# Performance work log

Measured on AMD Instinct MI355X. Metric: run time of the kernel, lower is better.

The kernel has to match this reference:

```python
import jax, jax.numpy as jnp
import numpy as np

B, T, D_MODEL, N_HEADS = 4, 2048, 1024, 16


def _alibi_bias(n_heads, seq_len):
    # matches torch alibi_bias(): slopes 2**(-8*i/m), i=1..m, m = pow2_ceil(n_heads)
    m = 1
    while m < n_heads:
        m *= 2
    slopes = jnp.array([2.0 ** (-8.0 * i / m) for i in range(1, m + 1)][:n_heads],
                       dtype=jnp.float32)
    pos = jnp.arange(seq_len)
    bias = (pos[None, :] - pos[:, None]).astype(jnp.float32)  # [T, T], j - i
    return slopes[:, None, None, None] * bias[None, None]      # [H, 1, T, T]


def setup_inputs() -> dict:
    key = jax.random.key(0)
    kx, kqkv, ko = jax.random.split(key, 3)
    x = jax.random.normal(kx, (B, T, D_MODEL), dtype=jnp.float32)
    Wqkv = jax.random.normal(kqkv, (3 * D_MODEL, D_MODEL), dtype=jnp.float32) / np.sqrt(D_MODEL)
    Wo = jax.random.normal(ko, (D_MODEL, D_MODEL), dtype=jnp.float32) / np.sqrt(D_MODEL)
    alibi = _alibi_bias(N_HEADS, T)  # [H, 1, T, T]
    return {"x": x, "alibi": alibi, "Wqkv": Wqkv, "Wo": Wo}


def reference(x, alibi, Wqkv, Wo):
    Bb, Tt, C = x.shape
    H = N_HEADS
    dk = C // H
    # qkv projection: [B, T, 3C] -> [B, T, 3, H, dk]
    qkv = (x @ Wqkv.T).reshape(Bb, Tt, 3, H, dk)
    q = jnp.moveaxis(qkv[:, :, 0], 2, 1)  # [B, H, T, dk]
    k = jnp.moveaxis(qkv[:, :, 1], 2, 1)
    v = jnp.moveaxis(qkv[:, :, 2], 2, 1)
    # causal (-inf above diagonal) + alibi additive mask, fp32, like the torch path
    causal = jnp.triu(jnp.full((Tt, Tt), -jnp.inf, dtype=jnp.float32), k=1)
    mask = causal[None, None] + alibi[:, 0][None]  # [1, H, T, T]
    scores = jnp.einsum('bhqd,bhkd->bhqk', q, k) / jnp.sqrt(jnp.float32(dk)) + mask
    p = jax.nn.softmax(scores, axis=-1)
    att = jnp.einsum('bhqk,bhkd->bhqd', p, v)           # [B, H, T, dk]
    y = jnp.moveaxis(att, 1, 2).reshape(Bb, Tt, C)       # [B, T, C]
    return y @ Wo.T
```

## Files before the change

kernel.cpp:

```cpp
#include <hip/hip_runtime.h>
#include <hip/hip_bf16.h>


#define B_ 4
#define T_ 2048
#define C_ 1024
#define H_ 16
#define DK 64

typedef __attribute__((ext_vector_type(8))) short short8;
typedef __attribute__((ext_vector_type(4))) float floatx4;

#define GLDS16(g, l)                                                          \
    __builtin_amdgcn_global_load_lds(                                         \
        (const __attribute__((address_space(1))) void*)(g),                   \
        (__attribute__((address_space(3))) void*)(l), 16, 0, 0)

static __device__ inline short f2bf(float x) {
    __hip_bfloat16 h = __float2bfloat16(x);
    return *reinterpret_cast<short*>(&h);
}

__global__ void detect_k(const unsigned int* __restrict__ x,
                         const unsigned int* __restrict__ ali,
                         const unsigned int* __restrict__ wqkv,
                         const unsigned int* __restrict__ wo,
                         int* __restrict__ flags) {
    __shared__ int cnt[4];
    const int tid = threadIdx.x;
    if (tid < 4) cnt[tid] = 0;
    __syncthreads();
    const int g = tid >> 6, l = tid & 63;
    const unsigned int* p = (g == 0) ? x : (g == 1) ? ali : (g == 2) ? wqkv : wo;
    int c = 0;
    for (int i = 0; i < 4; i++) {
        unsigned int w = p[l * 4 + i];
        int e0 = (w >> 7) & 0xFF;
        int e1 = (w >> 23) & 0xFF;
        c += (e0 >= 100 && e0 <= 140);
        c += (e1 >= 100 && e1 <= 140);
    }
    atomicAdd(&cnt[g], c);
    __syncthreads();
    if (l == 0) flags[g] = (cnt[g] < 400) ? 1 : 0;
}

__global__ void tobf16_all_k(const void* __restrict__ x,
                             const void* __restrict__ wq,
                             const void* __restrict__ wo,
                             short* __restrict__ ox,
                             short* __restrict__ owq,
                             short* __restrict__ owo) {
    const int bid = blockIdx.x;
    const void* in;
    short* out;
    int n8, b0, nb;
    if (bid < 2048) {
        in = x; out = ox; n8 = B_ * T_ * C_ / 8; b0 = bid; nb = 2048;
    } else if (bid < 3584) {
        in = wq; out = owq; n8 = 3 * C_ * C_ / 8; b0 = bid - 2048; nb = 1536;
    } else {
        in = wo; out = owo; n8 = C_ * C_ / 8; b0 = bid - 3584; nb = 512;
    }
    const unsigned int* u = (const unsigned int*)in;
    int c = 0;
#pragma unroll
    for (int i = 0; i < 16; i++) {
        unsigned int w = u[i];
        int e0 = (w >> 7) & 0xFF;
        int e1 = (w >> 23) & 0xFF;
        c += (e0 >= 100 && e0 <= 140);
        c += (e1 >= 100 && e1 <= 140);
    }
    const bool f32 = (c < 25);
    int i = b0 * blockDim.x + threadIdx.x;
    const int stride = nb * blockDim.x;
    for (; i < n8; i += stride) {
        if (f32) {
            float4 f0 = ((const float4*)in)[2 * i];
            float4 f1 = ((const float4*)in)[2 * i + 1];
            short8 v = { f2bf(f0.x), f2bf(f0.y), f2bf(f0.z), f2bf(f0.w),
                         f2bf(f1.x), f2bf(f1.y), f2bf(f1.z), f2bf(f1.w) };
            *(short8*)(out + (size_t)i * 8) = v;
        } else {
            *(short8*)(out + (size_t)i * 8) = ((const short8*)in)[i];
        }
    }
}

__global__ __launch_bounds__(256) void gemm_qkvvt_k(
    const short* __restrict__ xbf, const short* __restrict__ wqkvbf,
    short* __restrict__ qkv) {
    const int K = 1024;
    const int tid  = threadIdx.x;
    const int wv   = tid >> 6;
    const int lane = tid & 63;
    const int l15  = lane & 15;
    const int quad = lane >> 4;
    const int wm = wv >> 1, wn = wv & 1;

    const int id = blockIdx.x;
    const bool m0 = id < 1024;
    int bm, bn;
    const short *Ap, *Wp;
    if (m0) {
        bn = id & 15; bm = id >> 4; Ap = xbf; Wp = wqkvbf;
    } else {
        int j = id - 1024;
        bn = j & 63; bm = j >> 6;
        Ap = wqkvbf + (size_t)2048 * 1024; Wp = xbf;
    }

    __shared__ short As[128 * 64];
    __shared__ short Bs[128 * 64];

    floatx4 acc[4][4];
#pragma unroll
    for (int mt = 0; mt < 4; mt++)
#pragma unroll
        for (int nt = 0; nt < 4; nt++)
#pragma unroll
            for (int r = 0; r < 4; r++) acc[mt][nt][r] = 0.f;

    const int lr = lane >> 3;
    const int lc = lane & 7;
    const int cg = lc ^ lr;

    for (int kt = 0; kt < K; kt += 64) {
        __syncthreads();
#pragma unroll
        for (int i = 0; i < 4; i++) {
            const int rbase = wv * 32 + i * 8;
            const int r = rbase + lr;
            size_t ga = (size_t)(bm * 128 + r) * K + kt + cg * 8;
            GLDS16(Ap + ga, As + rbase * 64);
            size_t gb = (size_t)(bn * 128 + r) * K + kt + cg * 8;
            GLDS16(Wp + gb, Bs + rbase * 64);
        }
        __syncthreads();
#pragma unroll
        for (int ks = 0; ks < 64; ks += 32) {
            short8 af[4], bf[4];
#pragma unroll
            for (int mt = 0; mt < 4; mt++) {
                int row = wm * 64 + mt * 16 + l15;
                int cs = ((ks >> 3) + quad) ^ (row & 7);
                af[mt] = *(const short8*)(As + row * 64 + cs * 8);
            }
#pragma unroll
            for (int nt = 0; nt < 4; nt++) {
                int row = wn * 64 + nt * 16 + l15;
                int cs = ((ks >> 3) + quad) ^ (row & 7);
                bf[nt] = *(const short8*)(Bs + row * 64 + cs * 8);
            }
#pragma unroll
            for (int mt = 0; mt < 4; mt++)
#pragma unroll
                for (int nt = 0; nt < 4; nt++)
                    acc[mt][nt] = __builtin_amdgcn_mfma_f32_16x16x32_bf16(
                        af[mt], bf[nt], acc[mt][nt], 0, 0, 0);
        }
    }

#pragma unroll
    for (int mt = 0; mt < 4; mt++) {
#pragma unroll
        for (int nt = 0; nt < 4; nt++) {
#pragma unroll
            for (int r = 0; r < 4; r++) {
                int row = bm * 128 + wm * 64 + mt * 16 + quad * 4 + r;
                int col = bn * 128 + wn * 64 + nt * 16 + l15;
                if (m0) {
                    int b = row >> 11, t = row & (T_ - 1);
                    int s = col >> 10, rem = col & 1023;
                    int h = rem >> 6, d = rem & 63;
                    size_t dst = ((((size_t)s * B_ + b) * H_ + h) * T_ + t) * DK + d;
                    qkv[dst] = f2bf(acc[mt][nt][r]);
                } else {
                    int h = row >> 6, d = row & 63;
                    int b = col >> 11, t = col & (T_ - 1);
                    size_t dst = (((size_t)(2 * B_ + b) * H_ + h) * DK + d) * T_ + t;
                    qkv[dst] = f2bf(acc[mt][nt][r]);
                }
            }
        }
    }
}

template <int MODE, int N>
__global__ __launch_bounds__(256) void gemm128_k(const short* __restrict__ A,
                                                 const short* __restrict__ W,
                                                 void* __restrict__ Dv) {
    const int K = 1024;
    const int tid  = threadIdx.x;
    const int wv   = tid >> 6;
    const int lane = tid & 63;
    const int l15  = lane & 15;
    const int quad = lane >> 4;
    const int wm = wv >> 1, wn = wv & 1;
    const int bn = blockIdx.x, bm = blockIdx.y;

    __shared__ short As[128 * 64];
    __shared__ short Bs[128 * 64];

    floatx4 acc[4][4];
#pragma unroll
    for (int mt = 0; mt < 4; mt++)
#pragma unroll
        for (int nt = 0; nt < 4; nt++)
#pragma unroll
            for (int r = 0; r < 4; r++) acc[mt][nt][r] = 0.f;

    const int lr = lane >> 3;
    const int lc = lane & 7;
    const int cg = lc ^ lr;

    for (int kt = 0; kt < K; kt += 64) {
        __syncthreads();
#pragma unroll
        for (int i = 0; i < 4; i++) {
            const int rbase = wv * 32 + i * 8;
            const int r = rbase + lr;
            size_t ga;
            if (MODE == 2) {
                int rowg = bm * 128 + r;
                int b = rowg >> 11, t = rowg & (T_ - 1), hh = kt >> 6;
                ga = (((size_t)b * H_ + hh) * T_ + t) * DK + cg * 8;
            } else {
                ga = (size_t)(bm * 128 + r) * K + kt + cg * 8;
            }
            GLDS16(A + ga, As + rbase * 64);
            size_t gb = (size_t)(bn * 128 + r) * K + kt + cg * 8;
            GLDS16(W + gb, Bs + rbase * 64);
        }
        __syncthreads();
#pragma unroll
        for (int ks = 0; ks < 64; ks += 32) {
            short8 af[4], bf[4];
#pragma unroll
            for (int mt = 0; mt < 4; mt++) {
                int row = wm * 64 + mt * 16 + l15;
                int cs = ((ks >> 3) + quad) ^ (row & 7);
                af[mt] = *(const short8*)(As + row * 64 + cs * 8);
            }
#pragma unroll
            for (int nt = 0; nt < 4; nt++) {
                int row = wn * 64 + nt * 16 + l15;
                int cs = ((ks >> 3) + quad) ^ (row & 7);
                bf[nt] = *(const short8*)(Bs + row * 64 + cs * 8);
            }
#pragma unroll
            for (int mt = 0; mt < 4; mt++)
#pragma unroll
                for (int nt = 0; nt < 4; nt++)
                    acc[mt][nt] = __builtin_amdgcn_mfma_f32_16x16x32_bf16(
                        af[mt], bf[nt], acc[mt][nt], 0, 0, 0);
        }
    }

#pragma unroll
    for (int mt = 0; mt < 4; mt++) {
#pragma unroll
        for (int nt = 0; nt < 4; nt++) {
#pragma unroll
            for (int r = 0; r < 4; r++) {
                int row = bm * 128 + wm * 64 + mt * 16 + quad * 4 + r;
                int col = bn * 128 + wn * 64 + nt * 16 + l15;
                if (MODE == 0) {
                    int b = row >> 11, t = row & (T_ - 1);
                    int s = col >> 10, rem = col & 1023;
                    int h = rem >> 6, d = rem & 63;
                    size_t dst = ((((size_t)s * B_ + b) * H_ + h) * T_ + t) * DK + d;
                    ((short*)Dv)[dst] = f2bf(acc[mt][nt][r]);
                } else if (MODE == 3) {
                    int h = row >> 6, d = row & 63;
                    int b = col >> 11, t = col & (T_ - 1);
                    size_t dst = (((size_t)(2 * B_ + b) * H_ + h) * DK + d) * T_ + t;
                    ((short*)Dv)[dst] = f2bf(acc[mt][nt][r]);
                } else {
                    ((float*)Dv)[(size_t)row * N + col] = acc[mt][nt][r];
                }
            }
        }
    }
}

template <int MODE, int N>
__global__ __launch_bounds__(256) void gemm_k(const void* __restrict__ Av,
                                              const void* __restrict__ Wv,
                                              void* __restrict__ Dv,
                                              const int* fA, const int* fW,
                                              size_t aOff) {
    const int K = 1024;
    const int tid  = threadIdx.x;
    const int wave = tid >> 6;
    const int lane = tid & 63;
    const int l15  = lane & 15;
    const int quad = lane >> 4;
    const int bn = blockIdx.x;
    const int bm = blockIdx.y;
    const bool aF32 = fA && (*fA != 0);
    const bool wF32 = fW && (*fW != 0);

    __shared__ short As[64 * 72];
    __shared__ short Bs[64 * 72];

    floatx4 acc[4];
#pragma unroll
    for (int nt = 0; nt < 4; nt++)
#pragma unroll
        for (int r = 0; r < 4; r++) acc[nt][r] = 0.f;

    for (int kt = 0; kt < K; kt += 64) {
        __syncthreads();
#pragma unroll
        for (int i = 0; i < 2; i++) {
            int chunk = tid + i * 256;
            int r = chunk >> 3, c8 = (chunk & 7) * 8;
            size_t offA;
            if (MODE == 2) {
                int rowg = bm * 64 + r;
                int b = rowg >> 11, t = rowg & (T_ - 1), hh = kt >> 6;
                offA = (((size_t)b * H_ + hh) * T_ + t) * DK + c8;
            } else {
                offA = (size_t)(bm * 64 + r) * K + kt + c8;
            }
            size_t offW = (size_t)(bn * 64 + r) * K + kt + c8;
            if (aF32) {
                const float* Af = (const float*)Av + aOff;
                float4 f0 = *(const float4*)(Af + offA);
                float4 f1 = *(const float4*)(Af + offA + 4);
                short8 v = { f2bf(f0.x), f2bf(f0.y), f2bf(f0.z), f2bf(f0.w),
                             f2bf(f1.x), f2bf(f1.y), f2bf(f1.z), f2bf(f1.w) };
                *(short8*)(As + r * 72 + c8) = v;
            } else {
                *(short8*)(As + r * 72 + c8) =
                    *(const short8*)((const short*)Av + aOff + offA);
            }
            if (wF32) {
                const float* Wf = (const float*)Wv;
                float4 f0 = *(const float4*)(Wf + offW);
                float4 f1 = *(const float4*)(Wf + offW + 4);
                short8 v = { f2bf(f0.x), f2bf(f0.y), f2bf(f0.z), f2bf(f0.w),
                             f2bf(f1.x), f2bf(f1.y), f2bf(f1.z), f2bf(f1.w) };
                *(short8*)(Bs + r * 72 + c8) = v;
            } else {
                *(short8*)(Bs + r * 72 + c8) = *(const short8*)((const short*)Wv + offW);
            }
        }
        __syncthreads();
#pragma unroll
        for (int ks = 0; ks < 64; ks += 32) {
            short8 a = *(const short8*)(As + (wave * 16 + l15) * 72 + ks + quad * 8);
#pragma unroll
            for (int nt = 0; nt < 4; nt++) {
                short8 b = *(const short8*)(Bs + (nt * 16 + l15) * 72 + ks + quad * 8);
                acc[nt] = __builtin_amdgcn_mfma_f32_16x16x32_bf16(a, b, acc[nt], 0, 0, 0);
            }
        }
    }

#pragma unroll
    for (int nt = 0; nt < 4; nt++) {
#pragma unroll
        for (int r = 0; r < 4; r++) {
            int row = bm * 64 + wave * 16 + quad * 4 + r;
            int col = bn * 64 + nt * 16 + l15;
            if (MODE == 0) {
                int b = row >> 11, t = row & (T_ - 1);
                int s = col >> 10, rem = col & 1023;
                int h = rem >> 6, d = rem & 63;
                size_t dst = ((((size_t)s * B_ + b) * H_ + h) * T_ + t) * DK + d;
                ((short*)Dv)[dst] = f2bf(acc[nt][r]);
            } else if (MODE == 3) {
                int h = row >> 6, d = row & 63;
                int b = col >> 11, t = col & (T_ - 1);
                size_t dst = (((size_t)(2 * B_ + b) * H_ + h) * DK + d) * T_ + t;
                ((short*)Dv)[dst] = f2bf(acc[nt][r]);
            } else {
                ((float*)Dv)[(size_t)row * N + col] = acc[nt][r];
            }
        }
    }
}

__global__ __launch_bounds__(256, 4) void attn_k(short* __restrict__ qkv) {
    const int tid  = threadIdx.x;
    const int wave = tid >> 6;
    const int lane = tid & 63;
    const int l15  = lane & 15;
    const int quad = lane >> 4;
    const int gid  = blockIdx.x;
    const int bh = (gid & 7) * 8 + (gid >> 8);
    const int qb = (31 - ((gid >> 3) & 31)) * 64;
    const int b = bh >> 4, h = bh & 15;

    short* Qp       = qkv + (((size_t)(0 * B_ + b) * H_ + h) * T_) * DK;
    const short* Kp = qkv + (((size_t)(1 * B_ + b) * H_ + h) * T_) * DK;
    const short* Vt = qkv + (((size_t)(2 * B_ + b) * H_ + h) * DK) * T_;

    __shared__ short Ks[2][64 * 64];
    __shared__ short Vts[2][64 * 64];
    __shared__ short Ps[4 * 16 * 64];

    const size_t qrow = (size_t)(qb + wave * 16 + l15) * DK;
    const short8 aq0 = *(const short8*)(Qp + qrow + quad * 8);
    const short8 aq1 = *(const short8*)(Qp + qrow + 32 + quad * 8);

    const float LOG2E = 1.4426950408889634f;
    const float slope2 = exp2f(-0.5f * (float)(h + 1)) * LOG2E;
    const float scale2 = 0.125f * LOG2E;

    float lsum[4];
    floatx4 o[4];
#pragma unroll
    for (int r = 0; r < 4; r++) lsum[r] = 0.f;
#pragma unroll
    for (int nt = 0; nt < 4; nt++)
#pragma unroll
        for (int r = 0; r < 4; r++) o[nt][r] = 0.f;

    const int jt_end = qb >> 6;
    const int rb = qb + wave * 16 + quad * 4;
    int jstart = 0;
    {
        int lim = qb - 63 - (int)(50.f / slope2);
        if (lim > 0) jstart = lim >> 6;
    }

    const int lr = lane >> 3;
    const int cg = (lane & 7) ^ lr;

#pragma unroll
    for (int i = 0; i < 2; i++) {
        const int rbase = wave * 16 + i * 8;
        GLDS16(Kp + (size_t)(jstart * 64 + rbase + lr) * DK + cg * 8,
               &Ks[0][rbase * 64]);
        GLDS16(Vt + (size_t)(rbase + lr) * T_ + jstart * 64 + cg * 8,
               &Vts[0][rbase * 64]);
    }
    __syncthreads();

    floatx4 s[4];
#pragma unroll
    for (int nt = 0; nt < 4; nt++)
#pragma unroll
        for (int r = 0; r < 4; r++) s[nt][r] = 0.f;
    __builtin_amdgcn_s_setprio(1);
#pragma unroll
    for (int nt = 0; nt < 4; nt++) {
        int row = nt * 16 + l15;
        int c0 = quad ^ (row & 7);
        int c1 = (4 + quad) ^ (row & 7);
        short8 b0 = *(const short8*)(&Ks[0][0] + row * 64 + c0 * 8);
        short8 b1 = *(const short8*)(&Ks[0][0] + row * 64 + c1 * 8);
        s[nt] = __builtin_amdgcn_mfma_f32_16x16x32_bf16(aq0, b0, s[nt], 0, 0, 0);
        s[nt] = __builtin_amdgcn_mfma_f32_16x16x32_bf16(aq1, b1, s[nt], 0, 0, 0);
    }
    __builtin_amdgcn_s_setprio(0);

    int cur = 0;
    for (int jt = jstart; jt <= jt_end; jt++) {
        if (jt < jt_end) {
            const int nxt = cur ^ 1;
#pragma unroll
            for (int i = 0; i < 2; i++) {
                const int rbase = wave * 16 + i * 8;
                GLDS16(Kp + (size_t)((jt + 1) * 64 + rbase + lr) * DK + cg * 8,
                       &Ks[nxt][rbase * 64]);
                GLDS16(Vt + (size_t)(rbase + lr) * T_ + (jt + 1) * 64 + cg * 8,
                       &Vts[nxt][rbase * 64]);
            }
        }
        const short* Vtc = &Vts[cur][0];

        const bool diag = (jt == jt_end);
#pragma unroll
        for (int nt = 0; nt < 4; nt++) {
            int colg = jt * 64 + nt * 16 + l15;
            float cb = slope2 * (float)(colg - rb);
#pragma unroll
            for (int r = 0; r < 4; r++) {
                float sv = fmaf(s[nt][r], scale2, cb - slope2 * (float)r);
                if (diag && colg > rb + r) sv = -1e30f;
                float p = exp2f(sv);
                lsum[r] += p;
                int prow = quad * 4 + r;
                int pcol = nt * 16 + l15;
                Ps[wave * 1024 + prow * 64 +
                   (((pcol >> 3) ^ (prow & 7)) << 3) + (pcol & 7)] = f2bf(p);
            }
        }

        __builtin_amdgcn_s_setprio(1);
#pragma unroll
        for (int ks = 0; ks < 64; ks += 32) {
            short8 a = *(const short8*)(
                Ps + wave * 1024 + l15 * 64 +
                ((((ks >> 3) + quad) ^ (l15 & 7)) << 3));
#pragma unroll
            for (int nt = 0; nt < 4; nt++) {
                int row = nt * 16 + l15;
                int cs = ((ks >> 3) + quad) ^ (row & 7);
                short8 bf = *(const short8*)(Vtc + row * 64 + cs * 8);
                o[nt] = __builtin_amdgcn_mfma_f32_16x16x32_bf16(a, bf, o[nt], 0, 0, 0);
            }
        }
        __builtin_amdgcn_s_setprio(0);

        __syncthreads();
        cur ^= 1;

        if (jt < jt_end) {
            const short* Ksn = &Ks[cur][0];
#pragma unroll
            for (int nt = 0; nt < 4; nt++)
#pragma unroll
                for (int r = 0; r < 4; r++) s[nt][r] = 0.f;
            __builtin_amdgcn_s_setprio(1);
#pragma unroll
            for (int nt = 0; nt < 4; nt++) {
                int row = nt * 16 + l15;
                int c0 = quad ^ (row & 7);
                int c1 = (4 + quad) ^ (row & 7);
                short8 b0 = *(const short8*)(Ksn + row * 64 + c0 * 8);
                short8 b1 = *(const short8*)(Ksn + row * 64 + c1 * 8);
                s[nt] = __builtin_amdgcn_mfma_f32_16x16x32_bf16(aq0, b0, s[nt], 0, 0, 0);
                s[nt] = __builtin_amdgcn_mfma_f32_16x16x32_bf16(aq1, b1, s[nt], 0, 0, 0);
            }
            __builtin_amdgcn_s_setprio(0);
        }
    }

#pragma unroll
    for (int r = 0; r < 4; r++) {
#pragma unroll
        for (int mask = 1; mask < 16; mask <<= 1)
            lsum[r] += __shfl_xor(lsum[r], mask);
    }
#pragma unroll
    for (int nt = 0; nt < 4; nt++) {
#pragma unroll
        for (int r = 0; r < 4; r++) {
            int t = qb + wave * 16 + quad * 4 + r;
            int d = nt * 16 + l15;
            Qp[(size_t)t * DK + d] = f2bf(o[nt][r] / lsum[r]);
        }
    }
}

extern "C" void kernel_launch(void* const* d_in, const int* in_sizes, int n_in,
                              void* d_out, int out_size, void* d_ws, size_t ws_size,
                              hipStream_t stream) {
    const void* x    = d_in[0];
    const void* ali  = d_in[1];
    const void* Wqkv = d_in[2];
    const void* Wo   = d_in[3];
    float* out = (float*)d_out;

    int*   flags  = (int*)d_ws;
    short* qkv    = (short*)((char*)d_ws + 1024);
    short* xbf    = (short*)((char*)d_ws + 50332672);
    short* wqkvbf = (short*)((char*)d_ws + 67109888);
    short* wobf   = (short*)((char*)d_ws + 73401344);
    const bool fast = ws_size >= (size_t)75498496;

    dim3 blk(256);
    if (fast) {
        tobf16_all_k<<<4096, 256, 0, stream>>>(x, Wqkv, Wo, xbf, wqkvbf, wobf);
        gemm_qkvvt_k<<<1536, blk, 0, stream>>>(xbf, wqkvbf, qkv);
        attn_k<<<dim3(2048), blk, 0, stream>>>(qkv);
        gemm128_k<2, C_><<<dim3(8, 64), blk, 0, stream>>>(qkv, wobf, out);
    } else {
        detect_k<<<1, 256, 0, stream>>>((const unsigned int*)x,
                                        (const unsigned int*)ali,
                                        (const unsigned int*)Wqkv,
                                        (const unsigned int*)Wo, flags);
        gemm_k<0, 0><<<dim3(32, 128), blk, 0, stream>>>(x, Wqkv, qkv,
                                                        &flags[0], &flags[2], 0);
        gemm_k<3, 0><<<dim3(128, 16), blk, 0, stream>>>(Wqkv, x, qkv,
                                                        &flags[2], &flags[0],
                                                        (size_t)2048 * 1024);
        attn_k<<<dim3(2048), blk, 0, stream>>>(qkv);
        gemm_k<2, C_><<<dim3(16, 128), blk, 0, stream>>>(qkv, Wo, out,
                                                         nullptr, &flags[3], 0);
    }
}
```

Baseline: 521.2 us.

## Compute V with the plain QKV GEMM and transpose it in a separate kernel

The fused QKV GEMM no longer runs a second, operand-swapped GEMM to emit V already transposed. All of Q, K and V are now produced by one uniform GEMM, with a block-index swizzle meant to improve L2 reuse of the operand tiles. A new LDS-based transpose kernel then writes V^T into the now-unused xbf buffer, and attention reads V^T from there. This trades the strided transposed-output GEMM branch for an extra launch plus one more read and write pass over V.

```diff
diff --git a/kernel.cpp b/kernel.cpp
--- a/kernel.cpp
+++ b/kernel.cpp
@@ -88,7 +88,7 @@
     }
 }
 
-__global__ __launch_bounds__(256) void gemm_qkvvt_k(
+__global__ __launch_bounds__(256) void gemm_qkv_k(
     const short* __restrict__ xbf, const short* __restrict__ wqkvbf,
     short* __restrict__ qkv) {
     const int K = 1024;
@@ -99,17 +99,9 @@
     const int quad = lane >> 4;
     const int wm = wv >> 1, wn = wv & 1;
 
-    const int id = blockIdx.x;
-    const bool m0 = id < 1024;
-    int bm, bn;
-    const short *Ap, *Wp;
-    if (m0) {
-        bn = id & 15; bm = id >> 4; Ap = xbf; Wp = wqkvbf;
-    } else {
-        int j = id - 1024;
-        bn = j & 63; bm = j >> 6;
-        Ap = wqkvbf + (size_t)2048 * 1024; Wp = xbf;
-    }
+    const int id  = blockIdx.x;
+    const int swz = (id & 7) * 192 + (id >> 3);
+    const int bm = swz / 24, bn = swz % 24;
 
     __shared__ short As[128 * 64];
     __shared__ short Bs[128 * 64];
@@ -133,9 +125,9 @@
             const int rbase = wv * 32 + i * 8;
             const int r = rbase + lr;
             size_t ga = (size_t)(bm * 128 + r) * K + kt + cg * 8;
-            GLDS16(Ap + ga, As + rbase * 64);
+            GLDS16(xbf + ga, As + rbase * 64);
             size_t gb = (size_t)(bn * 128 + r) * K + kt + cg * 8;
-            GLDS16(Wp + gb, Bs + rbase * 64);
+            GLDS16(wqkvbf + gb, Bs + rbase * 64);
         }
         __syncthreads();
 #pragma unroll
@@ -170,21 +162,37 @@
             for (int r = 0; r < 4; r++) {
                 int row = bm * 128 + wm * 64 + mt * 16 + quad * 4 + r;
                 int col = bn * 128 + wn * 64 + nt * 16 + l15;
-                if (m0) {
-                    int b = row >> 11, t = row & (T_ - 1);
-                    int s = col >> 10, rem = col & 1023;
-                    int h = rem >> 6, d = rem & 63;
-                    size_t dst = ((((size_t)s * B_ + b) * H_ + h) * T_ + t) * DK + d;
-                    qkv[dst] = f2bf(acc[mt][nt][r]);
-                } else {
-                    int h = row >> 6, d = row & 63;
-                    int b = col >> 11, t = col & (T_ - 1);
-                    size_t dst = (((size_t)(2 * B_ + b) * H_ + h) * DK + d) * T_ + t;
-                    qkv[dst] = f2bf(acc[mt][nt][r]);
-                }
-            }
-        }
-    }
+                int b = row >> 11, t = row & (T_ - 1);
+                int s = col >> 10, rem = col & 1023;
+                int h = rem >> 6, d = rem & 63;
+                size_t dst = ((((size_t)s * B_ + b) * H_ + h) * T_ + t) * DK + d;
+                qkv[dst] = f2bf(acc[mt][nt][r]);
+            }
+        }
+    }
+}
+
+__global__ __launch_bounds__(256) void tr_k(const short* __restrict__ qkv,
+                                            short* __restrict__ vt) {
+    __shared__ short Ts[64][66];
+    const int gid = blockIdx.x;
+    const int bh = gid >> 5, tt = gid & 31;
+    const int b = bh >> 4, h = bh & 15;
+    const short* V = qkv + (((size_t)(2 * B_ + b) * H_ + h) * T_ + tt * 64) * DK;
+    short* D = vt + (((size_t)b * H_ + h) * DK) * T_ + tt * 64;
+    const int tid = threadIdx.x;
+    const int r = tid >> 2, c16 = (tid & 3) * 16;
+    *(short8*)&Ts[r][c16]     = *(const short8*)(V + (size_t)r * DK + c16);
+    *(short8*)&Ts[r][c16 + 8] = *(const short8*)(V + (size_t)r * DK + c16 + 8);
+    __syncthreads();
+    const int c = tid >> 2, r16 = (tid & 3) * 16;
+    short8 o0, o1;
+#pragma unroll
+    for (int i = 0; i < 8; i++) o0[i] = Ts[r16 + i][c];
+#pragma unroll
+    for (int i = 0; i < 8; i++) o1[i] = Ts[r16 + 8 + i][c];
+    *(short8*)(D + (size_t)c * T_ + r16)     = o0;
+    *(short8*)(D + (size_t)c * T_ + r16 + 8) = o1;
 }
 
 template <int MODE, int N>
@@ -384,7 +392,8 @@
     }
 }
 
-__global__ __launch_bounds__(256, 4) void attn_k(short* __restrict__ qkv) {
+__global__ __launch_bounds__(256, 4) void attn_k(short* __restrict__ qkv,
+                                                 const short* __restrict__ vtb) {
     const int tid  = threadIdx.x;
     const int wave = tid >> 6;
     const int lane = tid & 63;
@@ -397,7 +406,7 @@
 
     short* Qp       = qkv + (((size_t)(0 * B_ + b) * H_ + h) * T_) * DK;
     const short* Kp = qkv + (((size_t)(1 * B_ + b) * H_ + h) * T_) * DK;
-    const short* Vt = qkv + (((size_t)(2 * B_ + b) * H_ + h) * DK) * T_;
+    const short* Vt = vtb + (((size_t)b * H_ + h) * DK) * T_;
 
     __shared__ short Ks[2][64 * 64];
     __shared__ short Vts[2][64 * 64];
@@ -568,8 +577,9 @@
     dim3 blk(256);
     if (fast) {
         tobf16_all_k<<<4096, 256, 0, stream>>>(x, Wqkv, Wo, xbf, wqkvbf, wobf);
-        gemm_qkvvt_k<<<1536, blk, 0, stream>>>(xbf, wqkvbf, qkv);
-        attn_k<<<dim3(2048), blk, 0, stream>>>(qkv);
+        gemm_qkv_k<<<1536, blk, 0, stream>>>(xbf, wqkvbf, qkv);
+        tr_k<<<2048, blk, 0, stream>>>(qkv, xbf);
+        attn_k<<<dim3(2048), blk, 0, stream>>>(qkv, xbf);
         gemm128_k<2, C_><<<dim3(8, 64), blk, 0, stream>>>(qkv, wobf, out);
     } else {
         detect_k<<<1, 256, 0, stream>>>((const unsigned int*)x,
@@ -581,7 +591,8 @@
         gemm_k<3, 0><<<dim3(128, 16), blk, 0, stream>>>(Wqkv, x, qkv,
                                                         &flags[2], &flags[0],
                                                         (size_t)2048 * 1024);
-        attn_k<<<dim3(2048), blk, 0, stream>>>(qkv);
+        attn_k<<<dim3(2048), blk, 0, stream>>>(
+            qkv, qkv + (size_t)2 * B_ * H_ * T_ * DK);
         gemm_k<2, C_><<<dim3(16, 128), blk, 0, stream>>>(qkv, Wo, out,
                                                          nullptr, &flags[3], 0);
     }
```

After: 523.1 us. About the same (+0.4%).
